# Kernel tuning notes

Measured on AMD Instinct MI355X. Metric: run time of the kernel, lower is better.

The kernel has to match this reference:

```python
import jax, jax.numpy as jnp
import numpy as np

V, H, B, T_ENC, S, T_DEC, G = 18000, 400, 16, 256, 30, 8, 3


def setup_inputs() -> dict:
    key = jax.random.key(0)
    ks = jax.random.split(key, 16)
    def n(k, shape, s=0.1):
        return jax.random.normal(k, shape, jnp.float32) * s
    return {
        'story': jax.random.randint(ks[0], (B, T_ENC), 0, V, dtype=jnp.int32),
        'target_batches': jax.random.randint(ks[1], (B, S, T_DEC), 0, V, dtype=jnp.int32),
        'emb': n(ks[2], (V, H)),
        'enc_Wih_f': n(ks[3], (3 * H, H)), 'enc_Whh_f': n(ks[4], (3 * H, H)),
        'enc_bih_f': jnp.zeros((3 * H,), jnp.float32), 'enc_bhh_f': jnp.zeros((3 * H,), jnp.float32),
        'enc_Wih_b': n(ks[5], (3 * H, H)), 'enc_Whh_b': n(ks[6], (3 * H, H)),
        'enc_bih_b': jnp.zeros((3 * H,), jnp.float32), 'enc_bhh_b': jnp.zeros((3 * H,), jnp.float32),
        'dec_Wih': n(ks[7], (3 * H, H)), 'dec_Whh': n(ks[8], (3 * H, H)),
        'dec_bih': jnp.zeros((3 * H,), jnp.float32), 'dec_bhh': jnp.zeros((3 * H,), jnp.float32),
        'W_ratio': n(ks[9], (1, 3 * H)), 'b_ratio': jnp.zeros((1,), jnp.float32),
        'W_gate': n(ks[10], (G, H)), 'b_gate': jnp.zeros((G,), jnp.float32),
        'slot_emb': n(ks[11], (S, H)),
    }


def _gru_step(h, x, Wih, Whh, bih, bhh):
    # PyTorch GRU gate order: r, z, n
    gi = x @ Wih.T + bih
    gh = h @ Whh.T + bhh
    ir, iz, ig = jnp.split(gi, 3, axis=-1)
    hr, hz, hg = jnp.split(gh, 3, axis=-1)
    r = jax.nn.sigmoid(ir + hr)
    z = jax.nn.sigmoid(iz + hz)
    g = jnp.tanh(ig + r * hg)
    return (1.0 - z) * g + z * h


def _run_gru(xs, h0, Wih, Whh, bih, bhh):
    def step(h, x):
        h2 = _gru_step(h, x, Wih, Whh, bih, bhh)
        return h2, h2
    hT, out = jax.lax.scan(step, h0, xs)
    return out, hT


def reference(story, target_batches, emb,
              enc_Wih_f, enc_Whh_f, enc_bih_f, enc_bhh_f,
              enc_Wih_b, enc_Whh_b, enc_bih_b, enc_bhh_b,
              dec_Wih, dec_Whh, dec_bih, dec_bhh,
              W_ratio, b_ratio, W_gate, b_gate, slot_emb):
    # ---- EncoderRNN (bidirectional 1-layer GRU; dropout=0 / eval mode) ----
    x = emb[story.T]                       # (T_enc, B, H)
    h0 = jnp.zeros((B, H), x.dtype)
    out_f, h_f = _run_gru(x, h0, enc_Wih_f, enc_Whh_f, enc_bih_f, enc_bhh_f)
    out_b_rev, h_b = _run_gru(x[::-1], h0, enc_Wih_b, enc_Whh_b, enc_bih_b, enc_bhh_b)
    out_b = out_b_rev[::-1]
    enc_out = jnp.transpose(out_f + out_b, (1, 0, 2))   # (B, T_enc, H) = fwd+bwd halves summed
    enc_hidden = h_f + h_b                               # (B, H)     = hidden[0] + hidden[1]

    # ---- Generator decode loop ----
    SB = S * B
    dec_in0 = jnp.broadcast_to(slot_emb[:, None, :], (S, B, H)).reshape(SB, H)
    h = jnp.tile(enc_hidden, (S, 1))                     # (SB, H)
    enc_tiled = jnp.tile(enc_out, (S, 1, 1))             # (SB, T_enc, H)
    story_tiled = jnp.tile(story, (S, 1))                # (SB, T_enc)
    rows = jnp.arange(SB)[:, None]
    # teacher-forcing tokens per step, slot-major flatten to (T_dec, SB)
    tf_tokens = jnp.transpose(target_batches, (2, 1, 0)).reshape(T_DEC, SB)

    def step(carry, tok):
        h, dec_in = carry
        h2 = _gru_step(h, dec_in, dec_Wih, dec_Whh, dec_bih, dec_bhh)  # dec_state == new hidden
        scores = jnp.einsum('nd,ntd->nt', h2, enc_tiled)               # attend (all lens == T_enc)
        prob = jax.nn.softmax(scores, axis=1)
        context = jnp.einsum('nt,ntd->nd', prob, enc_tiled)
        gate = context @ W_gate.T + b_gate                              # (SB, G)
        p_vocab = jax.nn.softmax(h2 @ emb.T, axis=1)                    # (SB, V)
        p_gen = jnp.concatenate([h2, context, dec_in], axis=-1)         # (SB, 3H)
        sw = jax.nn.sigmoid(p_gen @ W_ratio.T + b_ratio)                # (SB, 1)
        ptr = jnp.zeros((SB, V), prob.dtype).at[rows, story_tiled].add(prob)  # scatter_add copy dist
        final = (1.0 - sw) * ptr + sw * p_vocab
        dec_in_next = emb[tok]                                          # teacher forcing
        return (h2, dec_in_next), (final, gate)

    _, (finals, gates) = jax.lax.scan(step, (h, dec_in0), tf_tokens)
    all_pointer_outputs = finals.reshape(T_DEC, S, B, V).transpose(1, 2, 0, 3)  # (S, B, T_dec, V)
    all_gate_outputs = gates[0].reshape(S, B, G)                                 # gate from step 0
    return all_pointer_outputs, all_gate_outputs
```

## Files before the change

kernel.cpp:

```cpp
#include <hip/hip_runtime.h>
#include <cstdint>
#include <cstddef>

#define VV 18000
#define HH 400
#define H3 1200
#define H3P 1280
#define KP 416
#define BB 16
#define TE 256
#define SS 30
#define TDN 8
#define GGN 3
#define SBN 480
#define NROW_ENC 4096
#define VP 18048
#define MP_DEC 512

#define EBLK 25
#define GIDEC_TILES 300
#define EMBB_BLKS 256

typedef __bf16 bf16;
typedef __attribute__((ext_vector_type(8))) __bf16 bf16x8;
typedef __attribute__((ext_vector_type(4))) float f32x4;
typedef __attribute__((ext_vector_type(4))) unsigned int u32x4;

static __device__ __forceinline__ float sigf(float x) {
    return 1.0f / (1.0f + __expf(-x));
}

static __device__ void gemm_dev(const bf16* __restrict__ A, const bf16* __restrict__ B,
                                float* __restrict__ Cf, bf16* __restrict__ Ch,
                                int M, int N, int K, int m0, int n0) {
    __shared__ __align__(16) bf16 sA[128 * 32];
    __shared__ __align__(16) bf16 sB[128 * 32];
    const int tid = threadIdx.x;
    const int lane = tid & 63;
    const int wave = tid >> 6;
    const int wm = wave >> 1, wn = wave & 1;
    f32x4 acc[4][4] = {};
    const int c0 = tid, c1 = tid + 256;
    const int r0 = c0 >> 2, q0 = (c0 & 3) * 8;
    const int r1 = c1 >> 2, q1 = (c1 & 3) * 8;
    const int ar = lane & 15, ak = (lane >> 4) * 8;
    const int nk = K >> 5;
    for (int kt = 0; kt < nk; ++kt) {
        const int kb = kt * 32;
        uint4 a0 = *(const uint4*)(A + (size_t)(m0 + r0) * K + kb + q0);
        uint4 a1 = *(const uint4*)(A + (size_t)(m0 + r1) * K + kb + q1);
        uint4 b0 = *(const uint4*)(B + (size_t)(n0 + r0) * K + kb + q0);
        uint4 b1 = *(const uint4*)(B + (size_t)(n0 + r1) * K + kb + q1);
        __syncthreads();
        *(uint4*)(sA + r0 * 32 + q0) = a0;
        *(uint4*)(sA + r1 * 32 + q1) = a1;
        *(uint4*)(sB + r0 * 32 + q0) = b0;
        *(uint4*)(sB + r1 * 32 + q1) = b1;
        __syncthreads();
        bf16x8 af[4], bg[4];
#pragma unroll
        for (int i = 0; i < 4; ++i)
            af[i] = *(const bf16x8*)(sA + (wm * 64 + i * 16 + ar) * 32 + ak);
#pragma unroll
        for (int j = 0; j < 4; ++j)
            bg[j] = *(const bf16x8*)(sB + (wn * 64 + j * 16 + ar) * 32 + ak);
#pragma unroll
        for (int i = 0; i < 4; ++i)
#pragma unroll
            for (int j = 0; j < 4; ++j)
                acc[i][j] = __builtin_amdgcn_mfma_f32_16x16x32_bf16(af[i], bg[j], acc[i][j], 0, 0, 0);
    }
    const int cr = (lane >> 4) * 4, cc = lane & 15;
    if (Ch) {
#pragma unroll
        for (int i = 0; i < 4; ++i)
#pragma unroll
            for (int j = 0; j < 4; ++j)
#pragma unroll
                for (int q = 0; q < 4; ++q) {
                    int row = m0 + wm * 64 + i * 16 + cr + q;
                    int col = n0 + wn * 64 + j * 16 + cc;
                    Ch[(size_t)row * N + col] = (bf16)acc[i][j][q];
                }
    } else {
#pragma unroll
        for (int i = 0; i < 4; ++i)
#pragma unroll
            for (int j = 0; j < 4; ++j)
#pragma unroll
                for (int q = 0; q < 4; ++q) {
                    int row = m0 + wm * 64 + i * 16 + cr + q;
                    int col = n0 + wn * 64 + j * 16 + cc;
                    Cf[(size_t)row * N + col] = acc[i][j][q];
                }
    }
}

__global__ __launch_bounds__(256) void gemm_bt(const bf16* __restrict__ A,
                                               const bf16* __restrict__ B,
                                               float* __restrict__ Cf, bf16* __restrict__ Ch,
                                               int M, int N, int K) {
    gemm_dev(A, B, Cf, Ch, M, N, K, blockIdx.x * 128, blockIdx.y * 128);
}

__global__ __launch_bounds__(256) void gemm_gi(const bf16* __restrict__ aenc,
                                               const bf16* __restrict__ wfb,
                                               const bf16* __restrict__ wbb,
                                               float* __restrict__ gif, float* __restrict__ gib) {
    const int dir = blockIdx.z;
    gemm_dev(aenc, dir ? wbb : wfb, dir ? gib : gif, nullptr,
             NROW_ENC, H3P, KP, blockIdx.x * 128, blockIdx.y * 128);
}

__global__ void prep_wpad4(const float* __restrict__ wih_f, const float* __restrict__ wih_b,
                           const float* __restrict__ dwih, const float* __restrict__ dwhh,
                           bf16* __restrict__ wfb, bf16* __restrict__ wbb,
                           bf16* __restrict__ dwihb, bf16* __restrict__ dwhhb) {
    int idx = blockIdx.x * blockDim.x + threadIdx.x;
    if (idx >= H3P * KP) return;
    int r = idx / KP, c = idx % KP;
    bool in = (r < H3 && c < HH);
    const float* src;
    bf16* dst;
    switch (blockIdx.y) {
        case 0: src = wih_f; dst = wfb; break;
        case 1: src = wih_b; dst = wbb; break;
        case 2: src = dwih; dst = dwihb; break;
        default: src = dwhh; dst = dwhhb; break;
    }
    dst[idx] = (bf16)(in ? src[(size_t)r * HH + c] : 0.f);
}

__global__ void prep_aenc(const int* __restrict__ story, const float* __restrict__ emb,
                          bf16* __restrict__ dst) {
    int idx = blockIdx.x * blockDim.x + threadIdx.x;
    if (idx >= NROW_ENC * KP) return;
    int m = idx / KP, k = idx % KP;
    int t = m >> 4, b = m & 15;
    float v = 0.f;
    if (k < HH) {
        int tok = story[b * TE + t];
        v = emb[(size_t)tok * HH + k];
    }
    dst[idx] = (bf16)v;
}

__global__ void prep_decx(const int* __restrict__ target, const float* __restrict__ emb,
                          const float* __restrict__ slot, float* __restrict__ xf,
                          bf16* __restrict__ xb) {
    int idx = blockIdx.x * blockDim.x + threadIdx.x;
    if (idx >= TDN * SBN * KP) return;
    int k = idx % KP;
    int nn = idx / KP;
    int n = nn % SBN;
    int td = nn / SBN;
    int s = n >> 4, b = n & 15;
    float v = 0.f;
    if (k < HH) {
        if (td == 0) v = slot[s * HH + k];
        else {
            int tok = target[(b * SS + s) * TDN + (td - 1)];
            v = emb[(size_t)tok * HH + k];
        }
        xf[((size_t)td * SBN + n) * HH + k] = v;
    }
    xb[idx] = (bf16)v;
}

__global__ void zero_bf16k(bf16* dst, size_t total) {
    size_t idx = (size_t)blockIdx.x * blockDim.x + threadIdx.x;
    if (idx < total) dst[idx] = (bf16)0.f;
}

__global__ __launch_bounds__(256) void enc_fat(
    const float* __restrict__ gi_f, const float* __restrict__ gi_b,
    const float* __restrict__ whh_f, const float* __restrict__ whh_b,
    const float* __restrict__ bih_f, const float* __restrict__ bhh_f,
    const float* __restrict__ bih_b, const float* __restrict__ bhh_b,
    float* __restrict__ hist_f, float* __restrict__ hist_b,
    unsigned int* __restrict__ hbuf_f, unsigned int* __restrict__ hbuf_b,
    unsigned int* __restrict__ flags,
    const bf16* __restrict__ decxb, const bf16* __restrict__ dwihb,
    float* __restrict__ gidec,
    const float* __restrict__ emb, bf16* __restrict__ embb) {
    const int bid = blockIdx.x;
    const int tid = threadIdx.x;

    if (bid >= 2 * EBLK) {
        if (bid < 2 * EBLK + GIDEC_TILES) {
            int t = bid - 2 * EBLK;
            gemm_dev(decxb, dwihb, gidec, nullptr, TDN * SBN, H3P, KP,
                     (t % 30) * 128, (t / 30) * 128);
        } else {
            const size_t total = (size_t)VP * KP;
            size_t idx = (size_t)(bid - 2 * EBLK - GIDEC_TILES) * 256 + tid;
            const size_t stride = (size_t)EMBB_BLKS * 256;
            for (; idx < total; idx += stride) {
                int r = (int)(idx / KP), c = (int)(idx % KP);
                float v = (r < VV && c < HH) ? emb[(size_t)r * HH + c] : 0.f;
                embb[idx] = (bf16)v;
            }
        }
        return;
    }

    const int dir = bid & 1;
    const int blk = bid >> 1;
    const int j0 = blk * 16;
    const float* gi  = dir ? gi_b : gi_f;
    const float* whh = dir ? whh_b : whh_f;
    const float* bih = dir ? bih_b : bih_f;
    const float* bhh = dir ? bhh_b : bhh_f;
    float* hist = dir ? hist_b : hist_f;
    unsigned int* hbuf = dir ? hbuf_b : hbuf_f;

    __shared__ float GHL[3 * 256];

    const int wv = tid >> 6, lane = tid & 63;
    const int ub = tid >> 4, ucol = tid & 15;
    const int uj = j0 + ucol;
    const float bihr = bih[uj], bihz = bih[HH + uj], bihg = bih[2 * HH + uj];
    const float bhhr = bhh[uj], bhhz = bhh[HH + uj], bhhg = bhh[2 * HH + uj];

    const int kk0 = (lane >> 4) * 8;
    bf16x8 Bf[13];
    if (wv < 3) {
        const int brow = wv * HH + j0 + (lane & 15);
#pragma unroll
        for (int ks = 0; ks < 13; ++ks) {
            bf16x8 v;
#pragma unroll
            for (int e = 0; e < 8; ++e) {
                int k = kk0 + ks * 32 + e;
                v[e] = (k < HH) ? (bf16)whh[(size_t)brow * HH + k] : (bf16)0.f;
            }
            Bf[ks] = v;
        }
    }

    union UV { unsigned int d[4]; bf16x8 v; };

    float hp = 0.f;

    for (int s = 0; s < TE; ++s) {
        const int tt = dir ? (TE - 1 - s) : s;
        const float* gir = gi + ((size_t)tt * BB + ub) * H3P;
        float gi0 = gir[uj];
        float gi1 = gir[HH + uj];
        float gi2 = gir[2 * HH + uj];

        f32x4 acc0 = {}, acc1 = {};
        if (s > 0) {
            if (wv == 0) {
                const unsigned int* fl = flags + ((size_t)dir * TE + (s - 1)) * 32;
                while (true) {
                    unsigned f = 1u;
                    if (lane < EBLK)
                        asm volatile("global_load_dword %0, %1, off sc0 sc1"
                                     : "=v"(f) : "v"(fl + lane));
                    asm volatile("s_waitcnt vmcnt(0)" ::: "memory");
                    if (__all((int)(f != 0u))) break;
                }
            }
            __syncthreads();
            if (wv < 3) {
                const int ttp = dir ? (tt + 1) : (tt - 1);
                const unsigned int* hrow =
                    hbuf + ((size_t)ttp * BB + (lane & 15)) * KP + kk0;
                u32x4 ua[13], ubv[13];
#pragma unroll
                for (int ks = 0; ks < 13; ++ks) {
                    asm volatile("global_load_dwordx4 %0, %1, off offset:%c2 sc0 sc1"
                                 : "=v"(ua[ks]) : "v"(hrow), "n"(ks * 128));
                    asm volatile("global_load_dwordx4 %0, %1, off offset:%c2 sc0 sc1"
                                 : "=v"(ubv[ks]) : "v"(hrow), "n"(ks * 128 + 16));
                }
                asm volatile("s_waitcnt vmcnt(0)" ::: "memory");
                __builtin_amdgcn_sched_barrier(0);
#pragma unroll
                for (int ks = 0; ks < 13; ++ks) {
                    u32x4 a = ua[ks], b = ubv[ks];
                    UV ah, al;
                    ah.d[0] = (a.x & 0xffffu) | (a.y << 16);
                    ah.d[1] = (a.z & 0xffffu) | (a.w << 16);
                    ah.d[2] = (b.x & 0xffffu) | (b.y << 16);
                    ah.d[3] = (b.z & 0xffffu) | (b.w << 16);
                    al.d[0] = (a.x >> 16) | (a.y & 0xffff0000u);
                    al.d[1] = (a.z >> 16) | (a.w & 0xffff0000u);
                    al.d[2] = (b.x >> 16) | (b.y & 0xffff0000u);
                    al.d[3] = (b.z >> 16) | (b.w & 0xffff0000u);
                    acc0 = __builtin_amdgcn_mfma_f32_16x16x32_bf16(ah.v, Bf[ks], acc0, 0, 0, 0);
                    acc1 = __builtin_amdgcn_mfma_f32_16x16x32_bf16(al.v, Bf[ks], acc1, 0, 0, 0);
                }
            }
        }
        if (wv < 3) {
            f32x4 at = acc0 + acc1;
            const int cb0 = wv * 256 + ((lane >> 4) * 4) * 16 + (lane & 15);
            GHL[cb0]      = at[0];
            GHL[cb0 + 16] = at[1];
            GHL[cb0 + 32] = at[2];
            GHL[cb0 + 48] = at[3];
        }
        __syncthreads();

        float ghr = GHL[tid];
        float ghz = GHL[256 + tid];
        float ghg = GHL[512 + tid];
        float r = sigf(gi0 + bihr + ghr + bhhr);
        float z = sigf(gi1 + bihz + ghz + bhhz);
        float g = tanhf(gi2 + bihg + r * (ghg + bhhg));
        float hn = (1.f - z) * g + z * hp;
        hp = hn;
        hist[((size_t)tt * BB + ub) * HH + uj] = hn;
        bf16 hi = (bf16)hn;
        bf16 lo = (bf16)(hn - (float)hi);
        unsigned int pk = (unsigned int)__builtin_bit_cast(unsigned short, hi)
                        | ((unsigned int)__builtin_bit_cast(unsigned short, lo) << 16);
        unsigned int* hw = hbuf + ((size_t)tt * BB + ub) * KP + uj;
        asm volatile("global_store_dword %0, %1, off sc0 sc1" :: "v"(hw), "v"(pk) : "memory");

        asm volatile("s_waitcnt vmcnt(0)" ::: "memory");
        __syncthreads();
        if (tid == 0) {
            unsigned int one = 1u;
            unsigned int* fw = flags + ((size_t)dir * TE + s) * 32 + blk;
            asm volatile("global_store_dword %0, %1, off sc0 sc1" :: "v"(fw), "v"(one) : "memory");
        }
    }
}

__global__ void combine_enc(const float* __restrict__ hf, const float* __restrict__ hb,
                            float* __restrict__ enc_out) {
    int idx = blockIdx.x * blockDim.x + threadIdx.x;
    if (idx >= BB * TE * HH) return;
    int hcol = idx % HH;
    int t = (idx / HH) % TE;
    int b = idx / (HH * TE);
    size_t src = ((size_t)t * BB + b) * HH + hcol;
    enc_out[idx] = hf[src] + hb[src];
}

__global__ void init_hdec2(const float* __restrict__ hf, const float* __restrict__ hb,
                           float* __restrict__ hdec, bf16* __restrict__ h2b) {
    int idx = blockIdx.x * blockDim.x + threadIdx.x;
    if (idx >= SBN * HH) return;
    int hcol = idx % HH;
    int n = idx / HH;
    int b = n & 15;
    float v = hf[((size_t)(TE - 1) * BB + b) * HH + hcol] + hb[((size_t)b) * HH + hcol];
    hdec[idx] = v;
    h2b[(size_t)n * KP + hcol] = (bf16)v;
}

__global__ void gru_dec2(const float* __restrict__ gi, const float* __restrict__ gh,
                         const float* __restrict__ bih, const float* __restrict__ bhh,
                         const float* __restrict__ hprev, float* __restrict__ hnew,
                         bf16* __restrict__ h2b) {
    int idx = blockIdx.x * blockDim.x + threadIdx.x;
    if (idx >= SBN * HH) return;
    int n = idx / HH, j = idx % HH;
    const float* gir = gi + (size_t)n * H3P;
    const float* ghr = gh + (size_t)n * H3P;
    float r = sigf(gir[j] + bih[j] + ghr[j] + bhh[j]);
    float z = sigf(gir[HH + j] + bih[HH + j] + ghr[HH + j] + bhh[HH + j]);
    float g = tanhf(gir[2 * HH + j] + bih[2 * HH + j] + r * (ghr[2 * HH + j] + bhh[2 * HH + j]));
    float hn = (1.f - z) * g + z * hprev[idx];
    hnew[idx] = hn;
    h2b[(size_t)n * KP + j] = (bf16)hn;
}

__global__ __launch_bounds__(256) void attn3(
    const float* __restrict__ hfall,
    const float* __restrict__ enc,
    const float* __restrict__ decxf,
    const float* __restrict__ Wr, const float* __restrict__ br,
    const float* __restrict__ Wg, const float* __restrict__ bg,
    float* __restrict__ probw,
    float* __restrict__ sww,
    float* __restrict__ outg) {
    const int b = blockIdx.x >> 1;
    const int half = blockIdx.x & 1;
    const int td = blockIdx.y;
    const int s0 = half * 15;
    const int tid = threadIdx.x;
    const int lane = tid & 63, wv = tid >> 6;

    __shared__ __align__(16) float h2L[15][HH];
    __shared__ __align__(16) float scL[15][TE];
    __shared__ __align__(16) float cxL[15][HH];

    const float* h2base = hfall + (size_t)(td + 1) * SBN * HH;
    for (int i = tid; i < 15 * HH; i += 256) {
        int j = i / HH, k = i % HH;
        int n = (s0 + j) * BB + b;
        h2L[j][k] = h2base[(size_t)n * HH + k];
    }
    __syncthreads();

    {
        float acc[15];
#pragma unroll
        for (int j = 0; j < 15; ++j) acc[j] = 0.f;
        const float4* er = (const float4*)(enc + ((size_t)b * TE + tid) * HH);
        for (int k4 = 0; k4 < HH / 4; ++k4) {
            float4 e = er[k4];
#pragma unroll
            for (int j = 0; j < 15; ++j) {
                float4 hv = *(const float4*)(&h2L[j][k4 * 4]);
                acc[j] += e.x * hv.x + e.y * hv.y + e.z * hv.z + e.w * hv.w;
            }
        }
#pragma unroll
        for (int j = 0; j < 15; ++j) scL[j][tid] = acc[j];
    }
    __syncthreads();

    for (int j = wv; j < 15; j += 4) {
        float v0 = scL[j][lane], v1 = scL[j][lane + 64];
        float v2 = scL[j][lane + 128], v3 = scL[j][lane + 192];
        float m = fmaxf(fmaxf(v0, v1), fmaxf(v2, v3));
        for (int d = 32; d; d >>= 1) m = fmaxf(m, __shfl_xor(m, d));
        v0 = __expf(v0 - m); v1 = __expf(v1 - m);
        v2 = __expf(v2 - m); v3 = __expf(v3 - m);
        float s = v0 + v1 + v2 + v3;
        for (int d = 32; d; d >>= 1) s += __shfl_xor(s, d);
        float inv = 1.f / s;
        scL[j][lane]       = v0 * inv;
        scL[j][lane + 64]  = v1 * inv;
        scL[j][lane + 128] = v2 * inv;
        scL[j][lane + 192] = v3 * inv;
    }
    __syncthreads();

    for (int i = tid; i < 15 * TE; i += 256) {
        int j = i / TE, t = i % TE;
        int n = (s0 + j) * BB + b;
        probw[((size_t)td * SBN + n) * TE + t] = scL[j][t];
    }

    {
        float cx0[15], cx1[15];
#pragma unroll
        for (int j = 0; j < 15; ++j) { cx0[j] = 0.f; cx1[j] = 0.f; }
        const int c0 = tid, c1 = tid + 256;
        const bool has2 = (c1 < HH);
        for (int t = 0; t < TE; t += 2) {
            const float* e0r = enc + ((size_t)b * TE + t) * HH;
            const float* e1r = e0r + HH;
            float e00 = e0r[c0], e01 = e1r[c0];
            float e10 = 0.f, e11 = 0.f;
            if (has2) { e10 = e0r[c1]; e11 = e1r[c1]; }
#pragma unroll
            for (int j = 0; j < 15; ++j) {
                float2 p = *(const float2*)(&scL[j][t]);
                cx0[j] += p.x * e00 + p.y * e01;
                cx1[j] += p.x * e10 + p.y * e11;
            }
        }
#pragma unroll
        for (int j = 0; j < 15; ++j) {
            cxL[j][c0] = cx0[j];
            if (has2) cxL[j][c1] = cx1[j];
        }
    }
    __syncthreads();

    for (int j = wv; j < 15; j += 4) {
        int n = (s0 + j) * BB + b;
        const float* dx = decxf + ((size_t)td * SBN + n) * HH;
        float a = 0.f;
        for (int k = lane; k < H3; k += 64) {
            float v = (k < HH) ? h2L[j][k]
                    : (k < 2 * HH) ? cxL[j][k - HH]
                    : dx[k - 2 * HH];
            a += v * Wr[k];
        }
        for (int d = 32; d; d >>= 1) a += __shfl_xor(a, d);
        if (lane == 0) sww[(size_t)td * SBN + n] = sigf(a + br[0]);
    }

    if (td == 0) {
        for (int j = wv; j < 15; j += 4) {
            int n = (s0 + j) * BB + b;
#pragma unroll
            for (int g = 0; g < GGN; ++g) {
                float a = 0.f;
                for (int k = lane; k < HH; k += 64) a += cxL[j][k] * Wg[g * HH + k];
                for (int d = 32; d; d >>= 1) a += __shfl_xor(a, d);
                if (lane == 0) outg[n * GGN + g] = a + bg[g];
            }
        }
    }
}

__global__ __launch_bounds__(1024) void smax_scatter3(
    const bf16* __restrict__ logitsH, const float* __restrict__ sw,
    const int* __restrict__ story, const float* __restrict__ probw,
    float* __restrict__ out, int td0) {
    int n = blockIdx.x, tid = threadIdx.x;
    int td = td0 + blockIdx.y;
    const bf16* lrow = logitsH + ((size_t)blockIdx.y * MP_DEC + n) * VP;
    const float* prow = probw + ((size_t)td * SBN + n) * TE;
    float swv = sw[(size_t)td * SBN + n];
    __shared__ float red[16];
    __shared__ float bc[2];
    float v[18];
    float mx = -1e30f;
#pragma unroll
    for (int i = 0; i < 18; ++i) {
        int c = tid + (i << 10);
        v[i] = (c < VV) ? (float)lrow[c] : -1e30f;
        mx = fmaxf(mx, v[i]);
    }
    for (int d = 32; d; d >>= 1) mx = fmaxf(mx, __shfl_xor(mx, d));
    if ((tid & 63) == 0) red[tid >> 6] = mx;
    __syncthreads();
    if (tid == 0) {
        float m2 = red[0];
        for (int w = 1; w < 16; ++w) m2 = fmaxf(m2, red[w]);
        bc[0] = m2;
    }
    __syncthreads();
    mx = bc[0];
    float s = 0.f;
#pragma unroll
    for (int i = 0; i < 18; ++i) {
        int c = tid + (i << 10);
        if (c < VV) { v[i] = __expf(v[i] - mx); s += v[i]; }
    }
    for (int d = 32; d; d >>= 1) s += __shfl_xor(s, d);
    if ((tid & 63) == 0) red[tid >> 6] = s;
    __syncthreads();
    if (tid == 0) {
        float s2 = 0.f;
        for (int w = 0; w < 16; ++w) s2 += red[w];
        bc[1] = s2;
    }
    __syncthreads();
    float scale = swv / bc[1];
    float* orow = out + ((size_t)n * TDN + td) * VV;
#pragma unroll
    for (int i = 0; i < 18; ++i) {
        int c = tid + (i << 10);
        if (c < VV) orow[c] = v[i] * scale;
    }
    __syncthreads();
    if (tid < TE) {
        int b = n & 15;
        int tok = story[b * TE + tid];
        float val = (1.f - swv) * prow[tid];
        atomicAdd(orow + tok, val);
    }
}

static inline int cdiv(long long a, long long b) { return (int)((a + b - 1) / b); }

extern "C" void kernel_launch(void* const* d_in, const int* in_sizes, int n_in,
                              void* d_out, int out_size, void* d_ws, size_t ws_size,
                              hipStream_t stream) {
    const int*   story  = (const int*)d_in[0];
    const int*   target = (const int*)d_in[1];
    const float* emb    = (const float*)d_in[2];
    const float* wih_f  = (const float*)d_in[3];
    const float* whh_f  = (const float*)d_in[4];
    const float* bih_f  = (const float*)d_in[5];
    const float* bhh_f  = (const float*)d_in[6];
    const float* wih_b  = (const float*)d_in[7];
    const float* whh_b  = (const float*)d_in[8];
    const float* bih_b  = (const float*)d_in[9];
    const float* bhh_b  = (const float*)d_in[10];
    const float* dwih   = (const float*)d_in[11];
    const float* dwhh   = (const float*)d_in[12];
    const float* dbih   = (const float*)d_in[13];
    const float* dbhh   = (const float*)d_in[14];
    const float* wr     = (const float*)d_in[15];
    const float* brr    = (const float*)d_in[16];
    const float* wgg    = (const float*)d_in[17];
    const float* bgg    = (const float*)d_in[18];
    const float* slot   = (const float*)d_in[19];
    float* out = (float*)d_out;

    char* wsb = (char*)d_ws;
    size_t off = 0;
    auto alloc = [&](size_t bytes) -> char* {
        char* p = wsb + off;
        off = (off + bytes + 255) & ~(size_t)255;
        return p;
    };
    bf16*  embb  = (bf16*)alloc((size_t)VP * KP * 2);
    bf16*  aenc  = (bf16*)alloc((size_t)NROW_ENC * KP * 2);
    bf16*  wfb   = (bf16*)alloc((size_t)H3P * KP * 2);
    bf16*  wbb   = (bf16*)alloc((size_t)H3P * KP * 2);
    bf16*  dwihb = (bf16*)alloc((size_t)H3P * KP * 2);
    bf16*  dwhhb = (bf16*)alloc((size_t)H3P * KP * 2);
    bf16*  decxb = (bf16*)alloc((size_t)TDN * SBN * KP * 2);
    bf16*  h2ball= (bf16*)alloc((size_t)9 * MP_DEC * KP * 2);
    unsigned int* hbuff = (unsigned int*)alloc((size_t)TE * BB * KP * 4);
    unsigned int* hbufb = (unsigned int*)alloc((size_t)TE * BB * KP * 4);
    unsigned int* flags = (unsigned int*)alloc((size_t)2 * TE * 32 * 4);
    float* gif   = (float*)alloc((size_t)NROW_ENC * H3P * 4);
    float* gib   = (float*)alloc((size_t)NROW_ENC * H3P * 4);
    float* gidec = (float*)alloc((size_t)TDN * SBN * H3P * 4);
    float* ghdec = (float*)alloc((size_t)MP_DEC * H3P * 4);
    float* histf = (float*)alloc((size_t)TE * BB * HH * 4);
    float* histb = (float*)alloc((size_t)TE * BB * HH * 4);
    float* encout= (float*)alloc((size_t)BB * TE * HH * 4);
    float* decxf = (float*)alloc((size_t)TDN * SBN * HH * 4);
    float* hfall = (float*)alloc((size_t)9 * SBN * HH * 4);
    float* probw = (float*)alloc((size_t)TDN * SBN * TE * 4);
    float* sww   = (float*)alloc((size_t)TDN * SBN * 4);
    bf16*  logitsH = (bf16*)alloc((size_t)MP_DEC * VP * 2);
    const size_t bigBytes = (size_t)TDN * MP_DEC * VP * 2;
    bf16* logitsAllH = nullptr;
    if (off + bigBytes + 256 <= ws_size) logitsAllH = (bf16*)alloc(bigBytes);
    (void)in_sizes; (void)n_in; (void)out_size;

    (void)hipMemsetAsync(flags, 0, (size_t)2 * TE * 32 * 4, stream);

    const int thr = 256;
    prep_aenc<<<cdiv((long long)NROW_ENC * KP, thr), thr, 0, stream>>>(story, emb, aenc);
    {
        dim3 g(cdiv((long long)H3P * KP, thr), 4);
        prep_wpad4<<<g, thr, 0, stream>>>(wih_f, wih_b, dwih, dwhh, wfb, wbb, dwihb, dwhhb);
    }
    prep_decx<<<cdiv((long long)TDN * SBN * KP, thr), thr, 0, stream>>>(target, emb, slot, decxf, decxb);
    zero_bf16k<<<cdiv((long long)9 * MP_DEC * KP, thr), thr, 0, stream>>>(h2ball, (size_t)9 * MP_DEC * KP);

    {
        dim3 g(NROW_ENC / 128, H3P / 128, 2);
        gemm_gi<<<g, 256, 0, stream>>>(aenc, wfb, wbb, gif, gib);
    }

    enc_fat<<<2 * EBLK + GIDEC_TILES + EMBB_BLKS, 256, 0, stream>>>(
        gif, gib, whh_f, whh_b, bih_f, bhh_f, bih_b, bhh_b,
        histf, histb, hbuff, hbufb, flags,
        decxb, dwihb, gidec, emb, embb);

    combine_enc<<<cdiv((long long)BB * TE * HH, thr), thr, 0, stream>>>(histf, histb, encout);
    init_hdec2<<<cdiv((long long)SBN * HH, thr), thr, 0, stream>>>(histf, histb, hfall, h2ball);

    for (int td = 0; td < TDN; ++td) {
        dim3 g(MP_DEC / 128, H3P / 128);
        gemm_bt<<<g, 256, 0, stream>>>(h2ball + (size_t)td * MP_DEC * KP, dwhhb, ghdec, nullptr,
                                       MP_DEC, H3P, KP);
        gru_dec2<<<cdiv((long long)SBN * HH, thr), thr, 0, stream>>>(
            gidec + (size_t)td * SBN * H3P, ghdec, dbih, dbhh,
            hfall + (size_t)td * SBN * HH,
            hfall + (size_t)(td + 1) * SBN * HH,
            h2ball + (size_t)(td + 1) * MP_DEC * KP);
    }

    if (logitsAllH) {
        dim3 g((TDN * MP_DEC) / 128, VP / 128);
        gemm_bt<<<g, 256, 0, stream>>>(h2ball + (size_t)MP_DEC * KP, embb, nullptr, logitsAllH,
                                       TDN * MP_DEC, VP, KP);
        {
            dim3 ga(32, TDN);
            attn3<<<ga, 256, 0, stream>>>(hfall, encout, decxf, wr, brr, wgg, bgg,
                                          probw, sww, out + (size_t)SBN * TDN * VV);
        }
        dim3 gs(SBN, TDN);
        smax_scatter3<<<gs, 1024, 0, stream>>>(logitsAllH, sww, story, probw, out, 0);
    } else {
        {
            dim3 ga(32, TDN);
            attn3<<<ga, 256, 0, stream>>>(hfall, encout, decxf, wr, brr, wgg, bgg,
                                          probw, sww, out + (size_t)SBN * TDN * VV);
        }
        for (int td = 0; td < TDN; ++td) {
            dim3 g(MP_DEC / 128, VP / 128);
            gemm_bt<<<g, 256, 0, stream>>>(h2ball + (size_t)(td + 1) * MP_DEC * KP, embb,
                                           nullptr, logitsH, MP_DEC, VP, KP);
            dim3 gs(SBN, 1);
            smax_scatter3<<<gs, 1024, 0, stream>>>(logitsH, sww, story, probw, out, td);
        }
    }
}
```

Measured before the change: 1.705 ms.

## Fuse decoder GRU steps into one persistent kernel with global flag barriers

```diff
diff --git a/kernel.cpp b/kernel.cpp
--- a/kernel.cpp
+++ b/kernel.cpp
@@ -20,6 +20,7 @@
 #define EBLK 25
 #define GIDEC_TILES 300
 #define EMBB_BLKS 256
+#define DCB 40
 
 typedef __bf16 bf16;
 typedef __attribute__((ext_vector_type(8))) __bf16 bf16x8;
@@ -28,6 +29,10 @@
 
 static __device__ __forceinline__ float sigf(float x) {
     return 1.0f / (1.0f + __expf(-x));
+}
+
+static __device__ __forceinline__ unsigned short bfbits(float v) {
+    return __builtin_bit_cast(unsigned short, (bf16)v);
 }
 
 static __device__ void gemm_dev(const bf16* __restrict__ A, const bf16* __restrict__ B,
@@ -353,21 +358,163 @@
     h2b[(size_t)n * KP + hcol] = (bf16)v;
 }
 
-__global__ void gru_dec2(const float* __restrict__ gi, const float* __restrict__ gh,
-                         const float* __restrict__ bih, const float* __restrict__ bhh,
-                         const float* __restrict__ hprev, float* __restrict__ hnew,
-                         bf16* __restrict__ h2b) {
-    int idx = blockIdx.x * blockDim.x + threadIdx.x;
-    if (idx >= SBN * HH) return;
-    int n = idx / HH, j = idx % HH;
-    const float* gir = gi + (size_t)n * H3P;
-    const float* ghr = gh + (size_t)n * H3P;
-    float r = sigf(gir[j] + bih[j] + ghr[j] + bhh[j]);
-    float z = sigf(gir[HH + j] + bih[HH + j] + ghr[HH + j] + bhh[HH + j]);
-    float g = tanhf(gir[2 * HH + j] + bih[2 * HH + j] + r * (ghr[2 * HH + j] + bhh[2 * HH + j]));
-    float hn = (1.f - z) * g + z * hprev[idx];
-    hnew[idx] = hn;
-    h2b[(size_t)n * KP + j] = (bf16)hn;
+__global__ __launch_bounds__(256) void dec_chain(
+    const bf16* __restrict__ dwhhb, const float* __restrict__ gidec,
+    const float* __restrict__ dbih, const float* __restrict__ dbhh,
+    bf16* __restrict__ h2ball, float* __restrict__ hfall,
+    float* __restrict__ ghdec, unsigned int* __restrict__ dflags) {
+    const int bid = blockIdx.x;
+    const int mrow = bid / 10, ncol = bid % 10;
+    const int m0 = mrow * 128, n0 = ncol * 128;
+    const int tid = threadIdx.x;
+    const int wv = tid >> 6, lane = tid & 63;
+
+    __shared__ __align__(16) bf16 sA[128 * 32];
+    __shared__ __align__(16) bf16 sB[128 * 32];
+    __shared__ __align__(16) float GHS[6 * H3];
+
+    const int c0i = tid, c1i = tid + 256;
+    const int r0 = c0i >> 2, q0 = (c0i & 3) * 8;
+    const int r1 = c1i >> 2, q1 = (c1i & 3) * 8;
+    const int ar = lane & 15, ak = (lane >> 4) * 8;
+    const int wm = wv >> 1, wn = wv & 1;
+
+    for (int td = 0; td < TDN; ++td) {
+        {
+            const bf16* A = h2ball + (size_t)td * MP_DEC * KP;
+            f32x4 acc[4][4] = {};
+#pragma unroll 1
+            for (int kt = 0; kt < 13; ++kt) {
+                const int kb = kt * 32;
+                u32x4 a0, a1;
+                const bf16* ap0 = A + (size_t)(m0 + r0) * KP + kb + q0;
+                const bf16* ap1 = A + (size_t)(m0 + r1) * KP + kb + q1;
+                asm volatile("global_load_dwordx4 %0, %1, off sc0 sc1" : "=v"(a0) : "v"(ap0));
+                asm volatile("global_load_dwordx4 %0, %1, off sc0 sc1" : "=v"(a1) : "v"(ap1));
+                uint4 b0 = *(const uint4*)(dwhhb + (size_t)(n0 + r0) * KP + kb + q0);
+                uint4 b1 = *(const uint4*)(dwhhb + (size_t)(n0 + r1) * KP + kb + q1);
+                __syncthreads();
+                asm volatile("s_waitcnt vmcnt(0)" ::: "memory");
+                __builtin_amdgcn_sched_barrier(0);
+                *(u32x4*)(sA + r0 * 32 + q0) = a0;
+                *(u32x4*)(sA + r1 * 32 + q1) = a1;
+                *(uint4*)(sB + r0 * 32 + q0) = b0;
+                *(uint4*)(sB + r1 * 32 + q1) = b1;
+                __syncthreads();
+                bf16x8 af[4], bg[4];
+#pragma unroll
+                for (int i = 0; i < 4; ++i)
+                    af[i] = *(const bf16x8*)(sA + (wm * 64 + i * 16 + ar) * 32 + ak);
+#pragma unroll
+                for (int j = 0; j < 4; ++j)
+                    bg[j] = *(const bf16x8*)(sB + (wn * 64 + j * 16 + ar) * 32 + ak);
+#pragma unroll
+                for (int i = 0; i < 4; ++i)
+#pragma unroll
+                    for (int j = 0; j < 4; ++j)
+                        acc[i][j] = __builtin_amdgcn_mfma_f32_16x16x32_bf16(af[i], bg[j], acc[i][j], 0, 0, 0);
+            }
+            const int cr = (lane >> 4) * 4, cc = lane & 15;
+#pragma unroll
+            for (int i = 0; i < 4; ++i)
+#pragma unroll
+                for (int j = 0; j < 4; ++j)
+#pragma unroll
+                    for (int q = 0; q < 4; ++q) {
+                        float v = acc[i][j][q];
+                        float* p = ghdec + (size_t)(m0 + wm * 64 + i * 16 + cr + q) * H3P
+                                 + (n0 + wn * 64 + j * 16 + cc);
+                        asm volatile("global_store_dword %0, %1, off sc0 sc1"
+                                     :: "v"(p), "v"(v) : "memory");
+                    }
+        }
+        asm volatile("s_waitcnt vmcnt(0)" ::: "memory");
+        __syncthreads();
+        if (tid == 0) {
+            unsigned one = 1u;
+            unsigned* fw = dflags + (size_t)(2 * td) * 64 + bid;
+            asm volatile("global_store_dword %0, %1, off sc0 sc1" :: "v"(fw), "v"(one) : "memory");
+        }
+        if (wv == 0) {
+            const unsigned* fl = dflags + (size_t)(2 * td) * 64;
+            while (true) {
+                unsigned f = 1u;
+                if (lane < DCB)
+                    asm volatile("global_load_dword %0, %1, off sc0 sc1" : "=v"(f) : "v"(fl + lane));
+                asm volatile("s_waitcnt vmcnt(0)" ::: "memory");
+                if (__all((int)(f != 0u))) break;
+            }
+        }
+        __syncthreads();
+
+        const float* gitd = gidec + (size_t)td * SBN * H3P;
+#pragma unroll 1
+        for (int pass = 0; pass < 2; ++pass) {
+            const int rbase = bid * 12 + pass * 6;
+            {
+                f32x4 tmp[8];
+#pragma unroll
+                for (int it = 0; it < 8; ++it) {
+                    int i4 = tid + it * 256;
+                    if (i4 < 6 * 300) {
+                        const float* gp = ghdec + (size_t)(rbase + i4 / 300) * H3P + (i4 % 300) * 4;
+                        asm volatile("global_load_dwordx4 %0, %1, off sc0 sc1"
+                                     : "=v"(tmp[it]) : "v"(gp));
+                    }
+                }
+                asm volatile("s_waitcnt vmcnt(0)" ::: "memory");
+                __builtin_amdgcn_sched_barrier(0);
+#pragma unroll
+                for (int it = 0; it < 8; ++it) {
+                    int i4 = tid + it * 256;
+                    if (i4 < 6 * 300)
+                        *(f32x4*)(&GHS[(i4 / 300) * H3 + (i4 % 300) * 4]) = tmp[it];
+                }
+            }
+            __syncthreads();
+#pragma unroll
+            for (int it = 0; it < 10; ++it) {
+                int i = tid + it * 256;
+                if (i < 6 * HH) {
+                    int r = i / HH, j = i % HH;
+                    int n = rbase + r;
+                    const float* gir = gitd + (size_t)n * H3P;
+                    float gh0 = GHS[r * H3 + j];
+                    float gh1 = GHS[r * H3 + HH + j];
+                    float gh2 = GHS[r * H3 + 2 * HH + j];
+                    float rr = sigf(gir[j] + dbih[j] + gh0 + dbhh[j]);
+                    float zz = sigf(gir[HH + j] + dbih[HH + j] + gh1 + dbhh[HH + j]);
+                    float gg = tanhf(gir[2 * HH + j] + dbih[2 * HH + j] + rr * (gh2 + dbhh[2 * HH + j]));
+                    float hp = hfall[(size_t)td * SBN * HH + (size_t)n * HH + j];
+                    float hn = (1.f - zz) * gg + zz * hp;
+                    hfall[(size_t)(td + 1) * SBN * HH + (size_t)n * HH + j] = hn;
+                    unsigned hb = (unsigned)bfbits(hn);
+                    const bf16* hp2 = h2ball + (size_t)(td + 1) * MP_DEC * KP + (size_t)n * KP + j;
+                    asm volatile("global_store_short %0, %1, off sc0 sc1"
+                                 :: "v"(hp2), "v"(hb) : "memory");
+                }
+            }
+            __syncthreads();
+        }
+        asm volatile("s_waitcnt vmcnt(0)" ::: "memory");
+        __syncthreads();
+        if (tid == 0) {
+            unsigned one = 1u;
+            unsigned* fw = dflags + (size_t)(2 * td + 1) * 64 + bid;
+            asm volatile("global_store_dword %0, %1, off sc0 sc1" :: "v"(fw), "v"(one) : "memory");
+        }
+        if (wv == 0) {
+            const unsigned* fl = dflags + (size_t)(2 * td + 1) * 64;
+            while (true) {
+                unsigned f = 1u;
+                if (lane < DCB)
+                    asm volatile("global_load_dword %0, %1, off sc0 sc1" : "=v"(f) : "v"(fl + lane));
+                asm volatile("s_waitcnt vmcnt(0)" ::: "memory");
+                if (__all((int)(f != 0u))) break;
+            }
+        }
+        __syncthreads();
+    }
 }
 
 __global__ __launch_bounds__(256) void attn3(
@@ -598,7 +745,8 @@
     bf16*  h2ball= (bf16*)alloc((size_t)9 * MP_DEC * KP * 2);
     unsigned int* hbuff = (unsigned int*)alloc((size_t)TE * BB * KP * 4);
     unsigned int* hbufb = (unsigned int*)alloc((size_t)TE * BB * KP * 4);
-    unsigned int* flags = (unsigned int*)alloc((size_t)2 * TE * 32 * 4);
+    unsigned int* flags = (unsigned int*)alloc((size_t)(2 * TE * 32 + 16 * 64) * 4);
+    unsigned int* dflags = flags + 2 * TE * 32;
     float* gif   = (float*)alloc((size_t)NROW_ENC * H3P * 4);
     float* gib   = (float*)alloc((size_t)NROW_ENC * H3P * 4);
     float* gidec = (float*)alloc((size_t)TDN * SBN * H3P * 4);
@@ -616,7 +764,7 @@
     if (off + bigBytes + 256 <= ws_size) logitsAllH = (bf16*)alloc(bigBytes);
     (void)in_sizes; (void)n_in; (void)out_size;
 
-    (void)hipMemsetAsync(flags, 0, (size_t)2 * TE * 32 * 4, stream);
+    (void)hipMemsetAsync(flags, 0, (size_t)(2 * TE * 32 + 16 * 64) * 4, stream);
 
     const int thr = 256;
     prep_aenc<<<cdiv((long long)NROW_ENC * KP, thr), thr, 0, stream>>>(story, emb, aenc);
@@ -640,16 +788,7 @@
     combine_enc<<<cdiv((long long)BB * TE * HH, thr), thr, 0, stream>>>(histf, histb, encout);
     init_hdec2<<<cdiv((long long)SBN * HH, thr), thr, 0, stream>>>(histf, histb, hfall, h2ball);
 
-    for (int td = 0; td < TDN; ++td) {
-        dim3 g(MP_DEC / 128, H3P / 128);
-        gemm_bt<<<g, 256, 0, stream>>>(h2ball + (size_t)td * MP_DEC * KP, dwhhb, ghdec, nullptr,
-                                       MP_DEC, H3P, KP);
-        gru_dec2<<<cdiv((long long)SBN * HH, thr), thr, 0, stream>>>(
-            gidec + (size_t)td * SBN * H3P, ghdec, dbih, dbhh,
-            hfall + (size_t)td * SBN * HH,
-            hfall + (size_t)(td + 1) * SBN * HH,
-            h2ball + (size_t)(td + 1) * MP_DEC * KP);
-    }
+    dec_chain<<<DCB, 256, 0, stream>>>(dwhhb, gidec, dbih, dbhh, h2ball, hfall, ghdec, dflags);
 
     if (logitsAllH) {
         dim3 g((TDN * MP_DEC) / 128, VP / 128);
```

New measurement: 1.933 ms. 1.13x slower.
